# Optimization experiments

Hardware: AMD Instinct MI355X
Metric: run time of the kernel (lower is better)

The kernel has to match this reference:

```python
import jax, jax.numpy as jnp
import numpy as np

N_NODES = 100000
NEG_SLOPE = 0.2


def gat_conv(x, edge_src, edge_dst, W, att_src, att_dst, bias):
    """PyG-style GATConv with heads=1. edge_src/edge_dst include self-loops.
    x: [N, F_in], W: [F_in, F_out], att_src/att_dst: [F_out], bias: [F_out].
    """
    n = x.shape[0]
    h = x @ W  # [N, F_out]
    a_src = h @ att_src  # [N]
    a_dst = h @ att_dst  # [N]
    e = jax.nn.leaky_relu(a_src[edge_src] + a_dst[edge_dst], NEG_SLOPE)  # [E]
    # segment softmax over edges sharing a destination node
    m = jax.ops.segment_max(e, edge_dst, num_segments=n)  # [N]; self-loops ensure no empty segment
    p = jnp.exp(e - m[edge_dst])
    denom = jax.ops.segment_sum(p, edge_dst, num_segments=n)  # [N]
    alpha = p / denom[edge_dst]  # [E]
    out = jax.ops.segment_sum(alpha[:, None] * h[edge_src], edge_dst, num_segments=n)
    return out + bias


def setup_inputs() -> dict:
    key = jax.random.key(0)
    ks = jax.random.split(key, 16)
    n, e = N_NODES, 1_600_000
    f_in, f_hid, f_out = 128, 64, 32
    x = jax.random.normal(ks[0], (n, f_in), dtype=jnp.float32)
    edge_index = jax.random.randint(ks[1], (2, e), 0, n, dtype=jnp.int32)

    def lin(k, fi, fo):
        return jax.random.normal(k, (fi, fo), dtype=jnp.float32) / np.sqrt(fi).astype(np.float32)

    def att(k, fo):
        return jax.random.normal(k, (fo,), dtype=jnp.float32) / np.sqrt(fo).astype(np.float32)

    return {
        "x": x, "edge_index": edge_index,
        "W1": lin(ks[2], f_in, f_hid), "as1": att(ks[3], f_hid), "ad1": att(ks[4], f_hid),
        "b1": jnp.zeros((f_hid,), jnp.float32),
        "W2": lin(ks[5], f_hid, f_hid), "as2": att(ks[6], f_hid), "ad2": att(ks[7], f_hid),
        "b2": jnp.zeros((f_hid,), jnp.float32),
        "W3": lin(ks[8], f_hid, f_out), "as3": att(ks[9], f_out), "ad3": att(ks[10], f_out),
        "b3": jnp.zeros((f_out,), jnp.float32),
    }


def reference(x, edge_index, W1, as1, ad1, b1, W2, as2, ad2, b2, W3, as3, ad3, b3):
    n = x.shape[0]
    # PyG GATConv default add_self_loops=True
    loops = jnp.arange(n, dtype=edge_index.dtype)
    src = jnp.concatenate([edge_index[0], loops])
    dst = jnp.concatenate([edge_index[1], loops])

    h1 = jax.nn.relu(gat_conv(x, src, dst, W1, as1, ad1, b1))
    h2 = jax.nn.relu(gat_conv(h1, src, dst, W2, as2, ad2, b2))
    out = gat_conv(h2, src, dst, W3, as3, ad3, b3)
    return (out, h1, h2)
```

## Files before the change

kernel.cpp:

```cpp
#include <hip/hip_runtime.h>
#include <hip/hip_bf16.h>

#define NEG_SLOPE 0.2f

typedef __attribute__((ext_vector_type(8))) short bf16x8;
typedef __attribute__((ext_vector_type(4))) float f32x4;

__device__ __forceinline__ unsigned short bf16bits(float f) {
    __hip_bfloat16 t = __float2bfloat16(f);
    return *reinterpret_cast<unsigned short*>(&t);
}

template <int FIN, int FOUT>
__global__ __launch_bounds__(256) void node_linear(
    const float* __restrict__ x, const float* __restrict__ W,
    const float* __restrict__ att_s, const float* __restrict__ att_d,
    __hip_bfloat16* __restrict__ h, float* __restrict__ a_s, float* __restrict__ a_d, int n)
{
    constexpr int RS = FIN + 8;
    __shared__ unsigned short xt[64 * RS];
    __shared__ unsigned short Wt[FOUT * RS];
    const int tid = threadIdx.x;
    const int base = blockIdx.x * 64;

    for (int i = tid; i < 64 * FIN / 2; i += 256) {
        int node = i / (FIN / 2);
        int k2 = i % (FIN / 2);
        float2 v = make_float2(0.f, 0.f);
        if (base + node < n) v = *(const float2*)(x + (size_t)(base + node) * FIN + k2 * 2);
        unsigned pk = (unsigned)bf16bits(v.x) | ((unsigned)bf16bits(v.y) << 16);
        *(unsigned*)(&xt[node * RS + k2 * 2]) = pk;
    }
    for (int i = tid; i < FIN * FOUT; i += 256) {
        int k = i / FOUT, f = i % FOUT;
        Wt[f * RS + k] = bf16bits(W[i]);
    }
    __syncthreads();

    const int wv = tid >> 6, lane = tid & 63;
    const int m = lane & 15, b = lane >> 4;
    const int node0 = base + wv * 16;

    float ps[4] = {0,0,0,0}, pd[4] = {0,0,0,0};
    #pragma unroll
    for (int t = 0; t < FOUT / 16; ++t) {
        f32x4 acc = {0.f, 0.f, 0.f, 0.f};
        #pragma unroll
        for (int ks = 0; ks < FIN / 32; ++ks) {
            bf16x8 a  = *(const bf16x8*)(&xt[(wv * 16 + m) * RS + ks * 32 + b * 8]);
            bf16x8 bb = *(const bf16x8*)(&Wt[(t * 16 + m) * RS + ks * 32 + b * 8]);
            acc = __builtin_amdgcn_mfma_f32_16x16x32_bf16(a, bb, acc, 0, 0, 0);
        }
        const float as_c = att_s[t * 16 + m];
        const float ad_c = att_d[t * 16 + m];
        #pragma unroll
        for (int r = 0; r < 4; ++r) {
            float v = acc[r];
            int node = node0 + b * 4 + r;
            if (node < n) h[(size_t)node * FOUT + t * 16 + m] = __float2bfloat16(v);
            ps[r] = fmaf(v, as_c, ps[r]);
            pd[r] = fmaf(v, ad_c, pd[r]);
        }
    }
    #pragma unroll
    for (int r = 0; r < 4; ++r) {
        float s = ps[r], d = pd[r];
        #pragma unroll
        for (int o = 8; o > 0; o >>= 1) { s += __shfl_xor(s, o); d += __shfl_xor(d, o); }
        int node = node0 + b * 4 + r;
        if (m == 0 && node < n) { a_s[node] = s; a_d[node] = d; }
    }
}


__global__ __launch_bounds__(256) void sb_hist(
    const int* __restrict__ edst, int E, int n, int* __restrict__ sbhist)
{
    __shared__ int lh[256];
    const int tid = threadIdx.x;
    lh[tid] = 0;
    __syncthreads();
    const int Etot = E + n;
    const int stride = gridDim.x * 256;
    for (int i = blockIdx.x * 256 + tid; i < Etot; i += stride) {
        int d = (i < E) ? edst[i] : i - E;
        atomicAdd(&lh[d >> 9], 1);
    }
    __syncthreads();
    if (lh[tid] > 0) atomicAdd(&sbhist[tid], lh[tid]);
}

__global__ __launch_bounds__(256) void sb_scan(
    const int* __restrict__ sbhist, int nsb, int Etot,
    int* __restrict__ sbbase, int* __restrict__ sbcur)
{
    __shared__ int buf[256];
    const int tid = threadIdx.x;
    int v = (tid < nsb) ? sbhist[tid] : 0;
    buf[tid] = v;
    __syncthreads();
    for (int off = 1; off < 256; off <<= 1) {
        int t = (tid >= off) ? buf[tid - off] : 0;
        __syncthreads();
        buf[tid] += t;
        __syncthreads();
    }
    if (tid < nsb) {
        int ex = buf[tid] - v;
        sbbase[tid] = ex;
        sbcur[tid] = ex;
    }
    if (tid == 0) sbbase[nsb] = Etot;
}

#define CB_CHUNK 4096
#define CB_NSB_MAX 256
__global__ __launch_bounds__(256) void chunk_bin(
    const int* __restrict__ esrc, const int* __restrict__ edst, int E, int n,
    int nsb, int* __restrict__ sbcur, int* __restrict__ packed1)
{
    __shared__ int pk[CB_CHUNK];
    __shared__ unsigned short sbv[CB_CHUNK];
    __shared__ int hist[CB_NSB_MAX];
    __shared__ int gbase[CB_NSB_MAX];
    const int tid = threadIdx.x;
    const int i0 = blockIdx.x * CB_CHUNK;
    const int Etot = E + n;

    hist[tid] = 0;
    __syncthreads();

    for (int j = tid; j < CB_CHUNK; j += 256) {
        int i = i0 + j;
        if (i < Etot) {
            int s, d;
            if (i < E) { s = esrc[i]; d = edst[i]; }
            else       { s = d = i - E; }
            int sb = d >> 9;
            pk[j] = ((d & 511) << 17) | s;
            sbv[j] = (unsigned short)sb;
            atomicAdd(&hist[sb], 1);
        } else {
            sbv[j] = 0xFFFFu;
        }
    }
    __syncthreads();

    if (tid < nsb && hist[tid] > 0)
        gbase[tid] = atomicAdd(&sbcur[tid], hist[tid]);
    hist[tid] = 0;
    __syncthreads();

    for (int j = tid; j < CB_CHUNK; j += 256) {
        unsigned short sb = sbv[j];
        if (sb != 0xFFFFu) {
            int pos = gbase[sb] + atomicAdd(&hist[sb], 1);
            packed1[pos] = pk[j];
        }
    }
}

__global__ __launch_bounds__(256) void sb_sort2(
    const int* __restrict__ sbbase, const int* __restrict__ packed1,
    int* __restrict__ col, int* __restrict__ row_end, int n)
{
    const int sb = blockIdx.x;
    const int node0 = sb << 9;
    const int lo = sbbase[sb];
    const int hi = sbbase[sb + 1];
    const int tid = threadIdx.x;
    __shared__ int c[512];
    __shared__ int sc[512];
    c[tid] = 0; c[tid + 256] = 0;
    __syncthreads();
    for (int j = lo + tid; j < hi; j += 256)
        atomicAdd(&c[((unsigned)packed1[j]) >> 17], 1);
    __syncthreads();
    sc[tid] = c[tid]; sc[tid + 256] = c[tid + 256];
    __syncthreads();
    for (int off = 1; off < 512; off <<= 1) {
        int i0 = tid, i1 = tid + 256;
        int v0 = (i0 >= off) ? sc[i0 - off] : 0;
        int v1 = (i1 >= off) ? sc[i1 - off] : 0;
        __syncthreads();
        sc[i0] += v0; sc[i1] += v1;
        __syncthreads();
    }
    #pragma unroll
    for (int q = 0; q < 2; ++q) {
        int i = tid + q * 256;
        int node = node0 + i;
        if (node < n) row_end[node] = lo + sc[i];
        c[i] = lo + sc[i] - c[i];
    }
    __syncthreads();
    for (int j = lo + tid; j < hi; j += 256) {
        int p = packed1[j];
        int ld = ((unsigned)p) >> 17;
        int pos = atomicAdd(&c[ld], 1);
        col[pos] = p & 0x1FFFF;
    }
}

template <int FOUT>
__global__ __launch_bounds__(256) void gat_aggregate(
    const int* __restrict__ row_end, const int* __restrict__ col,
    const float* __restrict__ a_s, const float* __restrict__ a_d,
    const __hip_bfloat16* __restrict__ h_, const float* __restrict__ bias,
    float* __restrict__ outp, int n, int do_relu)
{
    constexpr int LPN = FOUT / 4;
    constexpr int NPW = 64 / LPN;
    const unsigned short* h = (const unsigned short*)h_;
    const int gwave = (blockIdx.x * 256 + threadIdx.x) >> 6;
    const int lane = threadIdx.x & 63;
    const int node = gwave * NPW + lane / LPN;
    const int lsub = lane % LPN;
    if (node >= n) return;
    const int end = row_end[node];
    const int start = (node == 0) ? 0 : row_end[node - 1];
    const float adn = a_d[node];
    const int egrp = lane & ~(LPN - 1);
    float acc0 = 0.f, acc1 = 0.f, acc2 = 0.f, acc3 = 0.f, den = 0.f;
    for (int j = start; j < end; j += LPN) {
        int kmax = end - j; if (kmax > LPN) kmax = LPN;
        int k_idx = j + lsub;
        int sown = col[(k_idx < end) ? k_idx : (end - 1)];
        float eown = a_s[sown] + adn;
        eown = (eown > 0.f) ? eown : NEG_SLOPE * eown;
        float pown = (lsub < kmax) ? __expf(eown) : 0.f;
        for (int k = 0; k < kmax; ++k) {
            int   sk = __shfl(sown, egrp + k);
            float pk = __shfl(pown, egrp + k);
            den += pk;
            uint2 hv = *(const uint2*)(h + (size_t)sk * FOUT + lsub * 4);
            acc0 = fmaf(pk, __uint_as_float(hv.x << 16), acc0);
            acc1 = fmaf(pk, __uint_as_float(hv.x & 0xFFFF0000u), acc1);
            acc2 = fmaf(pk, __uint_as_float(hv.y << 16), acc2);
            acc3 = fmaf(pk, __uint_as_float(hv.y & 0xFFFF0000u), acc3);
        }
    }
    const float4 b4 = *(const float4*)(bias + lsub * 4);
    float inv = 1.f / den;
    float v0 = acc0 * inv + b4.x;
    float v1 = acc1 * inv + b4.y;
    float v2 = acc2 * inv + b4.z;
    float v3 = acc3 * inv + b4.w;
    if (do_relu) {
        v0 = fmaxf(v0, 0.f); v1 = fmaxf(v1, 0.f);
        v2 = fmaxf(v2, 0.f); v3 = fmaxf(v3, 0.f);
    }
    float4 o; o.x = v0; o.y = v1; o.z = v2; o.w = v3;
    *(float4*)(outp + (size_t)node * FOUT + lsub * 4) = o;
}

extern "C" void kernel_launch(void* const* d_in, const int* in_sizes, int n_in,
                              void* d_out, int out_size, void* d_ws, size_t ws_size,
                              hipStream_t stream)
{
    const float* x   = (const float*)d_in[0];
    const int* eidx  = (const int*)d_in[1];
    const float* W1  = (const float*)d_in[2];
    const float* as1 = (const float*)d_in[3];
    const float* ad1 = (const float*)d_in[4];
    const float* b1  = (const float*)d_in[5];
    const float* W2  = (const float*)d_in[6];
    const float* as2 = (const float*)d_in[7];
    const float* ad2 = (const float*)d_in[8];
    const float* b2  = (const float*)d_in[9];
    const float* W3  = (const float*)d_in[10];
    const float* as3 = (const float*)d_in[11];
    const float* ad3 = (const float*)d_in[12];
    const float* b3  = (const float*)d_in[13];

    const int fhid = in_sizes[3];
    const int fin  = in_sizes[2] / fhid;
    const int fo3  = in_sizes[11];
    const int n    = in_sizes[0] / fin;
    const int E    = in_sizes[1] / 2;
    const int Etot = E + n;
    const int nsb  = (n + 511) >> 9;

    const int* esrc = eidx;
    const int* edst = eidx + E;

    float* out = (float*)d_out;
    float* h1  = out + (size_t)n * fo3;
    float* h2  = h1 + (size_t)n * fhid;

    int* sbhist   = (int*)d_ws;
    int* sbbase   = sbhist + 256;
    int* sbcur    = sbbase + 260;
    int* row_end  = sbcur + 256;
    int* packed1  = row_end + n;
    int* col      = packed1 + Etot;
    __hip_bfloat16* h = (__hip_bfloat16*)(col + Etot);
    float* a_s    = (float*)(h + (size_t)n * fhid);
    float* a_d    = a_s + n;

    const int nchunks = (Etot + CB_CHUNK - 1) / CB_CHUNK;

    hipMemsetAsync(sbhist, 0, 256 * 4, stream);
    sb_hist<<<1024, 256, 0, stream>>>(edst, E, n, sbhist);
    sb_scan<<<1, 256, 0, stream>>>(sbhist, nsb, Etot, sbbase, sbcur);
    chunk_bin<<<nchunks, 256, 0, stream>>>(esrc, edst, E, n, nsb, sbcur, packed1);
    sb_sort2<<<nsb, 256, 0, stream>>>(sbbase, packed1, col, row_end, n);

    const int NLB = (n + 63) / 64;

    node_linear<128, 64><<<NLB, 256, 0, stream>>>(x, W1, as1, ad1, h, a_s, a_d, n);
    gat_aggregate<64><<<(n + 15) / 16, 256, 0, stream>>>(row_end, col, a_s, a_d, h, b1, h1, n, 1);

    node_linear<64, 64><<<NLB, 256, 0, stream>>>(h1, W2, as2, ad2, h, a_s, a_d, n);
    gat_aggregate<64><<<(n + 15) / 16, 256, 0, stream>>>(row_end, col, a_s, a_d, h, b2, h2, n, 1);

    node_linear<64, 32><<<NLB, 256, 0, stream>>>(h2, W3, as3, ad3, h, a_s, a_d, n);
    gat_aggregate<32><<<(n + 31) / 32, 256, 0, stream>>>(row_end, col, a_s, a_d, h, b3, out, n, 0);
}
```

Measured before the change: 292.6 us.

## Fuse next layer's linear projection and attention scores into aggregate epilogue

The aggregate kernel now stages each block's output rows in shared memory and computes the next layer's x@W product plus the a_src/a_dst dot products in an epilogue. It writes bf16 h and the score arrays into a second ping-pong workspace buffer. This removes two standalone node_linear launches and the re-read of h1/h2 from global memory. In exchange the epilogue uses fp32 FMA loops rather than MFMA, adds a block-wide barrier, and needs extra workspace; if the workspace is too small it falls back to the old path.

New measurement: 315.6 us. 7.9% more time.

```diff
diff --git a/kernel.cpp b/kernel.cpp
--- a/kernel.cpp
+++ b/kernel.cpp
@@ -202,26 +202,30 @@
     }
 }
 
-template <int FOUT>
+template <int FOUT, int NFOUT>
 __global__ __launch_bounds__(256) void gat_aggregate(
     const int* __restrict__ row_end, const int* __restrict__ col,
     const float* __restrict__ a_s, const float* __restrict__ a_d,
     const __hip_bfloat16* __restrict__ h_, const float* __restrict__ bias,
-    float* __restrict__ outp, int n, int do_relu)
+    float* __restrict__ outp, int n, int do_relu,
+    const float* __restrict__ Wn, const float* __restrict__ att_s_n,
+    const float* __restrict__ att_d_n, __hip_bfloat16* __restrict__ h_out,
+    float* __restrict__ a_s_out, float* __restrict__ a_d_out)
 {
     constexpr int LPN = FOUT / 4;
-    constexpr int NPW = 64 / LPN;
+    constexpr int NPB = 256 / LPN;
     const unsigned short* h = (const unsigned short*)h_;
-    const int gwave = (blockIdx.x * 256 + threadIdx.x) >> 6;
     const int lane = threadIdx.x & 63;
-    const int node = gwave * NPW + lane / LPN;
+    const int nl = (threadIdx.x >> 6) * (64 / LPN) + lane / LPN;
+    const int node = blockIdx.x * NPB + nl;
     const int lsub = lane % LPN;
-    if (node >= n) return;
-    const int end = row_end[node];
-    const int start = (node == 0) ? 0 : row_end[node - 1];
-    const float adn = a_d[node];
+    const bool active = (node < n);
+    const int end = active ? row_end[node] : 0;
+    const int start = (active && node > 0) ? row_end[node - 1] : 0;
+    const float adn = active ? a_d[node] : 0.f;
     const int egrp = lane & ~(LPN - 1);
-    float acc0 = 0.f, acc1 = 0.f, acc2 = 0.f, acc3 = 0.f, den = 0.f;
+    float acc0 = 0.f, acc1 = 0.f, acc2 = 0.f, acc3 = 0.f, den = 1.f;
+    if (active) den = 0.f;
     for (int j = start; j < end; j += LPN) {
         int kmax = end - j; if (kmax > LPN) kmax = LPN;
         int k_idx = j + lsub;
@@ -250,8 +254,49 @@
         v0 = fmaxf(v0, 0.f); v1 = fmaxf(v1, 0.f);
         v2 = fmaxf(v2, 0.f); v3 = fmaxf(v3, 0.f);
     }
-    float4 o; o.x = v0; o.y = v1; o.z = v2; o.w = v3;
-    *(float4*)(outp + (size_t)node * FOUT + lsub * 4) = o;
+    if (active) {
+        float4 o; o.x = v0; o.y = v1; o.z = v2; o.w = v3;
+        *(float4*)(outp + (size_t)node * FOUT + lsub * 4) = o;
+    }
+    if constexpr (NFOUT > 0) {
+        __shared__ float vs[NPB][FOUT + 4];
+        vs[nl][lsub * 4 + 0] = v0;
+        vs[nl][lsub * 4 + 1] = v1;
+        vs[nl][lsub * 4 + 2] = v2;
+        vs[nl][lsub * 4 + 3] = v3;
+        __syncthreads();
+        constexpr int FB = NFOUT / 4;
+        const int t = threadIdx.x;
+        if (t < NPB * FB) {
+            const int nl2 = t / FB, fb = t % FB;
+            const int node2 = blockIdx.x * NPB + nl2;
+            float g0 = 0.f, g1 = 0.f, g2 = 0.f, g3 = 0.f;
+            const float* wp = Wn + fb * 4;
+            #pragma unroll 4
+            for (int k = 0; k < FOUT; ++k) {
+                float xv = vs[nl2][k];
+                float4 w = *(const float4*)(wp + (size_t)k * NFOUT);
+                g0 = fmaf(xv, w.x, g0); g1 = fmaf(xv, w.y, g1);
+                g2 = fmaf(xv, w.z, g2); g3 = fmaf(xv, w.w, g3);
+            }
+            const float4 as4 = *(const float4*)(att_s_n + fb * 4);
+            const float4 ad4 = *(const float4*)(att_d_n + fb * 4);
+            float ps = g0 * as4.x + g1 * as4.y + g2 * as4.z + g3 * as4.w;
+            float pd = g0 * ad4.x + g1 * ad4.y + g2 * ad4.z + g3 * ad4.w;
+            #pragma unroll
+            for (int o = FB / 2; o > 0; o >>= 1) {
+                ps += __shfl_xor(ps, o);
+                pd += __shfl_xor(pd, o);
+            }
+            if (node2 < n) {
+                unsigned w0 = (unsigned)bf16bits(g0) | ((unsigned)bf16bits(g1) << 16);
+                unsigned w1 = (unsigned)bf16bits(g2) | ((unsigned)bf16bits(g3) << 16);
+                uint2 pk; pk.x = w0; pk.y = w1;
+                *(uint2*)((unsigned short*)h_out + (size_t)node2 * NFOUT + fb * 4) = pk;
+                if (fb == 0) { a_s_out[node2] = ps; a_d_out[node2] = pd; }
+            }
+        }
+    }
 }
 
 extern "C" void kernel_launch(void* const* d_in, const int* in_sizes, int n_in,
@@ -294,9 +339,13 @@
     int* row_end  = sbcur + 256;
     int* packed1  = row_end + n;
     int* col      = packed1 + Etot;
-    __hip_bfloat16* h = (__hip_bfloat16*)(col + Etot);
-    float* a_s    = (float*)(h + (size_t)n * fhid);
-    float* a_d    = a_s + n;
+    __hip_bfloat16* hA = (__hip_bfloat16*)(col + Etot);
+    float* a_sA   = (float*)(hA + (size_t)n * fhid);
+    float* a_dA   = a_sA + n;
+    __hip_bfloat16* hB = (__hip_bfloat16*)(a_dA + n);
+    float* a_sB   = (float*)(hB + (size_t)n * fhid);
+    float* a_dB   = a_sB + n;
+    size_t need_fused = (size_t)((char*)(a_dB + n) - (char*)d_ws);
 
     const int nchunks = (Etot + CB_CHUNK - 1) / CB_CHUNK;
 
@@ -307,13 +356,32 @@
     sb_sort2<<<nsb, 256, 0, stream>>>(sbbase, packed1, col, row_end, n);
 
     const int NLB = (n + 63) / 64;
-
-    node_linear<128, 64><<<NLB, 256, 0, stream>>>(x, W1, as1, ad1, h, a_s, a_d, n);
-    gat_aggregate<64><<<(n + 15) / 16, 256, 0, stream>>>(row_end, col, a_s, a_d, h, b1, h1, n, 1);
-
-    node_linear<64, 64><<<NLB, 256, 0, stream>>>(h1, W2, as2, ad2, h, a_s, a_d, n);
-    gat_aggregate<64><<<(n + 15) / 16, 256, 0, stream>>>(row_end, col, a_s, a_d, h, b2, h2, n, 1);
-
-    node_linear<64, 32><<<NLB, 256, 0, stream>>>(h2, W3, as3, ad3, h, a_s, a_d, n);
-    gat_aggregate<32><<<(n + 31) / 32, 256, 0, stream>>>(row_end, col, a_s, a_d, h, b3, out, n, 0);
-}
+    const int AGG64B = (n + 15) / 16;
+    const int AGG32B = (n + 31) / 32;
+
+    if (ws_size >= need_fused) {
+        node_linear<128, 64><<<NLB, 256, 0, stream>>>(x, W1, as1, ad1, hA, a_sA, a_dA, n);
+        gat_aggregate<64, 64><<<AGG64B, 256, 0, stream>>>(
+            row_end, col, a_sA, a_dA, hA, b1, h1, n, 1,
+            W2, as2, ad2, hB, a_sB, a_dB);
+        gat_aggregate<64, 32><<<AGG64B, 256, 0, stream>>>(
+            row_end, col, a_sB, a_dB, hB, b2, h2, n, 1,
+            W3, as3, ad3, hA, a_sA, a_dA);
+        gat_aggregate<32, 0><<<AGG32B, 256, 0, stream>>>(
+            row_end, col, a_sA, a_dA, hA, b3, out, n, 0,
+            nullptr, nullptr, nullptr, nullptr, nullptr, nullptr);
+    } else {
+        node_linear<128, 64><<<NLB, 256, 0, stream>>>(x, W1, as1, ad1, hA, a_sA, a_dA, n);
+        gat_aggregate<64, 0><<<AGG64B, 256, 0, stream>>>(
+            row_end, col, a_sA, a_dA, hA, b1, h1, n, 1,
+            nullptr, nullptr, nullptr, nullptr, nullptr, nullptr);
+        node_linear<64, 64><<<NLB, 256, 0, stream>>>(h1, W2, as2, ad2, hA, a_sA, a_dA, n);
+        gat_aggregate<64, 0><<<AGG64B, 256, 0, stream>>>(
+            row_end, col, a_sA, a_dA, hA, b2, h2, n, 1,
+            nullptr, nullptr, nullptr, nullptr, nullptr, nullptr);
+        node_linear<64, 32><<<NLB, 256, 0, stream>>>(h2, W3, as3, ad3, hA, a_sA, a_dA, n);
+        gat_aggregate<32, 0><<<AGG32B, 256, 0, stream>>>(
+            row_end, col, a_sA, a_dA, hA, b3, out, n, 0,
+            nullptr, nullptr, nullptr, nullptr, nullptr, nullptr);
+    }
+}
```
